# Kernel optimization log

Hardware: AMD Instinct MI355X
Metric: run time of the kernel (lower is better)

The kernel has to match this reference:

```python
import jax, jax.numpy as jnp
import numpy as np

N_NODES = 100000
N_EDGES = 3200000
F_IN = 512
F_HID = 16
F_OUT = 40


def setup_inputs() -> dict:
    key = jax.random.key(0)
    k_x, k_e, k_w1, k_w2 = jax.random.split(key, 4)
    x = jax.random.normal(k_x, (N_NODES, F_IN), dtype=jnp.float32)
    edge_index = jax.random.randint(k_e, (2, N_EDGES), 0, N_NODES, dtype=jnp.int32)
    # Glorot-ish init for GCN weights
    W1 = jax.random.normal(k_w1, (F_IN, F_HID), dtype=jnp.float32) * (1.0 / np.sqrt(F_IN))
    b1 = jnp.zeros((F_HID,), dtype=jnp.float32)
    W2 = jax.random.normal(k_w2, (F_HID, F_OUT), dtype=jnp.float32) * (1.0 / np.sqrt(F_HID))
    b2 = jnp.zeros((F_OUT,), dtype=jnp.float32)
    return {"x": x, "edge_index": edge_index, "W1": W1, "b1": b1, "W2": W2, "b2": b2}


def reference(x, edge_index, W1, b1, W2, b2):
    # Eval-mode forward: dropout is identity.
    n = x.shape[0]
    loops = jnp.arange(n, dtype=edge_index.dtype)
    row = jnp.concatenate([edge_index[0], loops])  # sources (incl. self-loops)
    col = jnp.concatenate([edge_index[1], loops])  # targets
    # Symmetric GCN normalization: deg^{-1/2}[row] * deg^{-1/2}[col]
    deg = jax.ops.segment_sum(jnp.ones_like(row, dtype=x.dtype), col, num_segments=n)
    dinv = jnp.where(deg > 0, jax.lax.rsqrt(deg), 0.0).astype(x.dtype)
    norm = dinv[row] * dinv[col]  # [E+N]

    def gcn_conv(h, W, b):
        h = h @ W                                   # [N, F_out] dense transform first
        msg = h[row] * norm[:, None]                # gather + scale
        return jax.ops.segment_sum(msg, col, num_segments=n) + b  # scatter-add

    h = jax.nn.relu(gcn_conv(x, W1, b1))
    out = gcn_conv(h, W2, b2)
    return jax.nn.log_softmax(out, axis=1)
```

## Files before the change

kernel.cpp:

```cpp
#include <hip/hip_runtime.h>
#include <hip/hip_bf16.h>

#define F_IN  512
#define F_HID 16
#define F_OUT 40
#define CH    8192

typedef __attribute__((ext_vector_type(4))) float f32x4;
typedef __attribute__((ext_vector_type(8))) short s16x8;
typedef unsigned short ushort_t;
typedef unsigned int uint_t;

__device__ __forceinline__ float lof(uint_t v) { return __uint_as_float(v << 16); }
__device__ __forceinline__ float hif(uint_t v) { return __uint_as_float(v & 0xffff0000u); }
__device__ __forceinline__ ushort_t f2bf(float f) {
    __hip_bfloat16 h = __float2bfloat16(f);
    union { __hip_bfloat16 h; ushort_t u; } v; v.h = h; return v.u;
}


__global__ __launch_bounds__(1024) void k_bhist(const int* __restrict__ col,
                                                int* __restrict__ bhall, int nE) {
    __shared__ int bh[256];
    int t = threadIdx.x;
    if (t < 256) bh[t] = 0;
    __syncthreads();
    int base = blockIdx.x * CH;
    int end  = min(base + CH, nE);
    for (int e = base + t; e < end; e += 1024)
        atomicAdd(&bh[col[e] >> 9], 1);
    __syncthreads();
    if (t < 256) bhall[blockIdx.x * 256 + t] = bh[t];
}

__global__ void k_bscan2(const int* __restrict__ bhall, int* __restrict__ bstart,
                         int* __restrict__ bcur, int nwge) {
    __shared__ int s[256];
    int t = threadIdx.x;
    int sum = 0;
    for (int w = 0; w < nwge; ++w) sum += bhall[w * 256 + t];
    s[t] = sum;
    __syncthreads();
    for (int off = 1; off < 256; off <<= 1) {
        int v = (t >= off) ? s[t - off] : 0;
        __syncthreads();
        s[t] += v;
        __syncthreads();
    }
    int ex = s[t] - sum;
    bstart[t] = ex;
    bcur[t] = ex;
    if (t == 255) bstart[256] = s[255];
}

__global__ __launch_bounds__(1024) void k_bscatter(const int* __restrict__ row,
                                                   const int* __restrict__ colv,
                                                   int* __restrict__ bcur,
                                                   int* __restrict__ pairs, int nE) {
    __shared__ int colS[CH];
    __shared__ int bh[256];
    __shared__ int lcur[256];
    int t = threadIdx.x;
    if (t < 256) bh[t] = 0;
    __syncthreads();
    int base = blockIdx.x * CH;
    int end  = min(base + CH, nE);
    for (int e = base + t; e < end; e += 1024) {
        int c = colv[e];
        colS[e - base] = c;
        atomicAdd(&bh[c >> 9], 1);
    }
    __syncthreads();
    if (t < 256) {
        int v = bh[t];
        if (v) lcur[t] = atomicAdd(&bcur[t], v);
    }
    __syncthreads();
    for (int e = base + t; e < end; e += 1024) {
        int c = colS[e - base];
        int pos = atomicAdd(&lcur[c >> 9], 1);
        pairs[pos] = (row[e] << 9) | (c & 511);
    }
}

__global__ __launch_bounds__(1024) void k_build(const int* __restrict__ bstart,
                                                const int* __restrict__ pairs,
                                                int* __restrict__ start,
                                                int* __restrict__ csr,
                                                float* __restrict__ dinv,
                                                int n, int nE) {
    __shared__ int h[512];
    __shared__ int s[512];
    __shared__ int cur[512];
    int t = threadIdx.x;
    if (t < 512) h[t] = 0;
    __syncthreads();
    int s0 = bstart[blockIdx.x], s1 = bstart[blockIdx.x + 1];
    for (int e = s0 + t; e < s1; e += 1024)
        atomicAdd(&h[pairs[e] & 511], 1);
    __syncthreads();
    if (t < 512) s[t] = h[t];
    __syncthreads();
    for (int off = 1; off < 512; off <<= 1) {
        int v = 0;
        if (t < 512 && t >= off) v = s[t - off];
        __syncthreads();
        if (t < 512) s[t] += v;
        __syncthreads();
    }
    if (t < 512) {
        int c = h[t];
        int st = s0 + s[t] - c;
        int node = (blockIdx.x << 9) + t;
        if (node < n) {
            start[node] = st;
            dinv[node] = rsqrtf((float)c + 1.0f);
        }
        cur[t] = st;
    }
    if (blockIdx.x == 0 && t == 0) start[n] = nE;
    __syncthreads();
    for (int e = s0 + t; e < s1; e += 1024) {
        int v = pairs[e];
        int pos = atomicAdd(&cur[v & 511], 1);
        csr[pos] = v >> 9;
    }
}

__global__ __launch_bounds__(256) void k_xw1(const float* __restrict__ x,
                                             const float* __restrict__ W1,
                                             const float* __restrict__ dinv,
                                             ushort_t* __restrict__ g1b, int n_tiles) {
    int lane = threadIdx.x & 63;
    int wid  = threadIdx.x >> 6;
    int m = lane & 15;
    int g = lane >> 4;

    s16x8 bf[16];
#pragma unroll
    for (int kb = 0; kb < 16; ++kb) {
        union { s16x8 s; unsigned u[4]; } bu;
#pragma unroll
        for (int p = 0; p < 4; ++p) {
            int k0 = kb * 32 + g * 8 + p * 2;
            float lo = W1[(k0 + 0) * F_HID + m];
            float hi = W1[(k0 + 1) * F_HID + m];
            unsigned pk;
            asm("v_cvt_pk_bf16_f32 %0, %1, %2" : "=v"(pk) : "v"(lo), "v"(hi));
            bu.u[p] = pk;
        }
        bf[kb] = bu.s;
    }

    int tile = blockIdx.x * 4 + wid;
    if (tile >= n_tiles) return;

    const float* xr = x + (size_t)(tile * 16 + m) * F_IN + g * 8;
    f32x4 acc = {0.f, 0.f, 0.f, 0.f};
#pragma unroll
    for (int kb = 0; kb < 16; ++kb) {
        f32x4 xa = *(const f32x4*)(xr + kb * 32);
        f32x4 xb = *(const f32x4*)(xr + kb * 32 + 4);
        union { s16x8 s; unsigned u[4]; } au;
        asm("v_cvt_pk_bf16_f32 %0, %1, %2" : "=v"(au.u[0]) : "v"(xa.x), "v"(xa.y));
        asm("v_cvt_pk_bf16_f32 %0, %1, %2" : "=v"(au.u[1]) : "v"(xa.z), "v"(xa.w));
        asm("v_cvt_pk_bf16_f32 %0, %1, %2" : "=v"(au.u[2]) : "v"(xb.x), "v"(xb.y));
        asm("v_cvt_pk_bf16_f32 %0, %1, %2" : "=v"(au.u[3]) : "v"(xb.z), "v"(xb.w));
        acc = __builtin_amdgcn_mfma_f32_16x16x32_bf16(au.s, bf[kb], acc, 0, 0, 0);
    }
#pragma unroll
    for (int p = 0; p < 4; ++p) {
        int rr = tile * 16 + g * 4 + p;
        g1b[(size_t)rr * F_HID + m] = f2bf(acc[p] * dinv[rr]);
    }
}

__global__ __launch_bounds__(256) void k_gather1(const int* __restrict__ start,
                                                 const int* __restrict__ csr,
                                                 const uint_t* __restrict__ g1,
                                                 const float* __restrict__ dinv,
                                                 const float* __restrict__ b1,
                                                 uint_t* __restrict__ g2, int n) {
    int wid = threadIdx.x >> 6, lane = threadIdx.x & 63;
    int node = blockIdx.x * 4 + wid;
    if (node >= n) return;
    int fp = lane & 7, sub = lane >> 3;
    int s0 = start[node], s1 = start[node + 1];
    int len = s1 - s0;
    int q = (len + 7) >> 3;
    int e = s0 + sub * q;
    int end = min(e + q, s1);
    float l0 = 0.f, h0 = 0.f, l1 = 0.f, h1 = 0.f, l2 = 0.f, h2 = 0.f, l3 = 0.f, h3 = 0.f;
    for (; e + 4 <= end; e += 4) {
        int r0 = csr[e], r1 = csr[e + 1], r2 = csr[e + 2], r3 = csr[e + 3];
        uint_t v0 = g1[r0 * 8 + fp], v1 = g1[r1 * 8 + fp];
        uint_t v2 = g1[r2 * 8 + fp], v3 = g1[r3 * 8 + fp];
        l0 += lof(v0); h0 += hif(v0);
        l1 += lof(v1); h1 += hif(v1);
        l2 += lof(v2); h2 += hif(v2);
        l3 += lof(v3); h3 += hif(v3);
    }
    for (; e < end; ++e) {
        uint_t v = g1[csr[e] * 8 + fp];
        l0 += lof(v); h0 += hif(v);
    }
    float alo = (l0 + l1) + (l2 + l3);
    float ahi = (h0 + h1) + (h2 + h3);
    alo += __shfl_xor(alo, 8);  ahi += __shfl_xor(ahi, 8);
    alo += __shfl_xor(alo, 16); ahi += __shfl_xor(ahi, 16);
    alo += __shfl_xor(alo, 32); ahi += __shfl_xor(ahi, 32);
    uint_t sv = g1[(size_t)node * 8 + fp];
    alo += lof(sv); ahi += hif(sv);
    float di = dinv[node];
    const float2* b1v = (const float2*)b1;
    float2 bb = b1v[fp];
    float hlo = fmaxf(di * alo + bb.x, 0.f) * di;
    float hhi = fmaxf(di * ahi + bb.y, 0.f) * di;
    if (sub == 0) {
        unsigned pk;
        asm("v_cvt_pk_bf16_f32 %0, %1, %2" : "=v"(pk) : "v"(hlo), "v"(hhi));
        g2[(size_t)node * 8 + fp] = pk;
    }
}

__global__ __launch_bounds__(256) void k_gather2f(const int* __restrict__ start,
                                                  const int* __restrict__ csr,
                                                  const uint_t* __restrict__ g2,
                                                  const float* __restrict__ dinv,
                                                  const float* __restrict__ W2,
                                                  const float* __restrict__ b2,
                                                  float* __restrict__ out, int n) {
    int wid = threadIdx.x >> 6, lane = threadIdx.x & 63;
    int node = blockIdx.x * 4 + wid;
    if (node >= n) return;
    int fp = lane & 7, sub = lane >> 3;
    int j = (lane < F_OUT) ? lane : 0;

    float w2c[F_HID];
#pragma unroll
    for (int k = 0; k < F_HID; ++k) w2c[k] = W2[k * F_OUT + j];
    float bj = b2[j];

    int s0 = start[node], s1 = start[node + 1];
    int len = s1 - s0;
    int q = (len + 7) >> 3;
    int e = s0 + sub * q;
    int end = min(e + q, s1);
    float l0 = 0.f, h0 = 0.f, l1 = 0.f, h1 = 0.f, l2 = 0.f, h2 = 0.f, l3 = 0.f, h3 = 0.f;
    for (; e + 4 <= end; e += 4) {
        int r0 = csr[e], r1 = csr[e + 1], r2 = csr[e + 2], r3 = csr[e + 3];
        uint_t v0 = g2[r0 * 8 + fp], v1 = g2[r1 * 8 + fp];
        uint_t v2 = g2[r2 * 8 + fp], v3 = g2[r3 * 8 + fp];
        l0 += lof(v0); h0 += hif(v0);
        l1 += lof(v1); h1 += hif(v1);
        l2 += lof(v2); h2 += hif(v2);
        l3 += lof(v3); h3 += hif(v3);
    }
    for (; e < end; ++e) {
        uint_t v = g2[csr[e] * 8 + fp];
        l0 += lof(v); h0 += hif(v);
    }
    float alo = (l0 + l1) + (l2 + l3);
    float ahi = (h0 + h1) + (h2 + h3);
    alo += __shfl_xor(alo, 8);  ahi += __shfl_xor(ahi, 8);
    alo += __shfl_xor(alo, 16); ahi += __shfl_xor(ahi, 16);
    alo += __shfl_xor(alo, 32); ahi += __shfl_xor(ahi, 32);
    uint_t sv = g2[(size_t)node * 8 + fp];
    alo += lof(sv); ahi += hif(sv);
    float di = dinv[node];
    float a_lo = di * alo;
    float a_hi = di * ahi;

    float o = bj;
#pragma unroll
    for (int k = 0; k < F_HID; k += 2) {
        o += __shfl(a_lo, k >> 1) * w2c[k] + __shfl(a_hi, k >> 1) * w2c[k + 1];
    }

    float mo = (lane < F_OUT) ? o : -3.4e38f;
#pragma unroll
    for (int off = 32; off; off >>= 1) mo = fmaxf(mo, __shfl_xor(mo, off));
    float ev = (lane < F_OUT) ? __expf(o - mo) : 0.f;
    float sv2 = ev;
#pragma unroll
    for (int off = 32; off; off >>= 1) sv2 += __shfl_xor(sv2, off);
    float lse = mo + __logf(sv2);
    if (lane < F_OUT) out[(size_t)node * F_OUT + lane] = o - lse;
}


extern "C" void kernel_launch(void* const* d_in, const int* in_sizes, int n_in,
                              void* d_out, int out_size, void* d_ws, size_t ws_size,
                              hipStream_t stream) {
    const float* x  = (const float*)d_in[0];
    const int*   ei = (const int*)d_in[1];
    const float* W1 = (const float*)d_in[2];
    const float* b1 = (const float*)d_in[3];
    const float* W2 = (const float*)d_in[4];
    const float* b2 = (const float*)d_in[5];
    float* out = (float*)d_out;

    const int N = out_size / F_OUT;
    const int E = in_sizes[1] / 2;
    const int* row = ei;
    const int* col = ei + E;

    const int NBUCK = (N + 511) >> 9;
    const int NWGE  = (E + CH - 1) / CH;
    const int tiles = (N + 15) / 16;
    const int nbT   = (tiles + 3) / 4;
    const int nbG   = (N + 3) / 4;

    int* bstart   = (int*)d_ws;
    int* bcur     = bstart + 260;
    int* bhall    = bcur + 256;
    int* start    = bhall + NWGE * 256;
    int* csr      = start + N + 4;
    int* pairs    = csr + E;
    float* dinv   = (float*)(pairs + E);
    uint_t* g1    = (uint_t*)(dinv + N);
    uint_t* g2    = g1 + (size_t)N * 8;

    k_bhist<<<NWGE, 1024, 0, stream>>>(col, bhall, E);
    k_bscan2<<<1, 256, 0, stream>>>(bhall, bstart, bcur, NWGE);
    k_bscatter<<<NWGE, 1024, 0, stream>>>(row, col, bcur, pairs, E);
    k_build<<<NBUCK, 1024, 0, stream>>>(bstart, pairs, start, csr, dinv, N, E);

    k_xw1<<<nbT, 256, 0, stream>>>(x, W1, dinv, (ushort_t*)g1, tiles);

    k_gather1<<<nbG, 256, 0, stream>>>(start, csr, g1, dinv, b1, g2, N);
    k_gather2f<<<nbG, 256, 0, stream>>>(start, csr, g2, dinv, W2, b2, out, N);
}
```

Measured before the change: 257.6 us.

## Fuse X@W1 with edge histogram and apply dinv scaling in CSR build

Merges the dense X@W1 MFMA kernel into the first histogram launch, so the bandwidth-heavy transform of x runs alongside the edge-bucket histogram instead of after the CSR build. The dinv scaling of g1 moves into k_build, which rescales the bf16 rows in place. The two gather kernels become persistent, with a fixed grid of 2048 blocks and each wave looping over a contiguous run of nodes, reusing start[] boundaries between nodes. The in-place rescale adds a second bf16 rounding, and the persistent split can unbalance work when degrees vary.

```diff
diff --git a/kernel.cpp b/kernel.cpp
--- a/kernel.cpp
+++ b/kernel.cpp
@@ -18,19 +18,67 @@
     union { __hip_bfloat16 h; ushort_t u; } v; v.h = h; return v.u;
 }
 
-
-__global__ __launch_bounds__(1024) void k_bhist(const int* __restrict__ col,
-                                                int* __restrict__ bhall, int nE) {
+__global__ __launch_bounds__(512) void k_pre(const float* __restrict__ x,
+                                             const float* __restrict__ W1,
+                                             ushort_t* __restrict__ g1b,
+                                             const int* __restrict__ col,
+                                             int* __restrict__ bhall,
+                                             int n_tiles, int nbX, int nE) {
     __shared__ int bh[256];
     int t = threadIdx.x;
-    if (t < 256) bh[t] = 0;
-    __syncthreads();
-    int base = blockIdx.x * CH;
-    int end  = min(base + CH, nE);
-    for (int e = base + t; e < end; e += 1024)
-        atomicAdd(&bh[col[e] >> 9], 1);
-    __syncthreads();
-    if (t < 256) bhall[blockIdx.x * 256 + t] = bh[t];
+    if ((int)blockIdx.x < nbX) {
+        int lane = t & 63;
+        int wid  = t >> 6;
+        int m = lane & 15;
+        int g = lane >> 4;
+        int tile = blockIdx.x * 8 + wid;
+        if (tile >= n_tiles) return;
+
+        s16x8 bf[16];
+#pragma unroll
+        for (int kb = 0; kb < 16; ++kb) {
+            union { s16x8 s; unsigned u[4]; } bu;
+#pragma unroll
+            for (int p = 0; p < 4; ++p) {
+                int k0 = kb * 32 + g * 8 + p * 2;
+                float lo = W1[(k0 + 0) * F_HID + m];
+                float hi = W1[(k0 + 1) * F_HID + m];
+                unsigned pk;
+                asm("v_cvt_pk_bf16_f32 %0, %1, %2" : "=v"(pk) : "v"(lo), "v"(hi));
+                bu.u[p] = pk;
+            }
+            bf[kb] = bu.s;
+        }
+
+        const float* xr = x + (size_t)(tile * 16 + m) * F_IN + g * 8;
+        f32x4 acc = {0.f, 0.f, 0.f, 0.f};
+#pragma unroll
+        for (int kb = 0; kb < 16; ++kb) {
+            f32x4 xa = *(const f32x4*)(xr + kb * 32);
+            f32x4 xb = *(const f32x4*)(xr + kb * 32 + 4);
+            union { s16x8 s; unsigned u[4]; } au;
+            asm("v_cvt_pk_bf16_f32 %0, %1, %2" : "=v"(au.u[0]) : "v"(xa.x), "v"(xa.y));
+            asm("v_cvt_pk_bf16_f32 %0, %1, %2" : "=v"(au.u[1]) : "v"(xa.z), "v"(xa.w));
+            asm("v_cvt_pk_bf16_f32 %0, %1, %2" : "=v"(au.u[2]) : "v"(xb.x), "v"(xb.y));
+            asm("v_cvt_pk_bf16_f32 %0, %1, %2" : "=v"(au.u[3]) : "v"(xb.z), "v"(xb.w));
+            acc = __builtin_amdgcn_mfma_f32_16x16x32_bf16(au.s, bf[kb], acc, 0, 0, 0);
+        }
+#pragma unroll
+        for (int p = 0; p < 4; ++p) {
+            int rr = tile * 16 + g * 4 + p;
+            g1b[(size_t)rr * F_HID + m] = f2bf(acc[p]);
+        }
+    } else {
+        int b = blockIdx.x - nbX;
+        if (t < 256) bh[t] = 0;
+        __syncthreads();
+        int base = b * CH;
+        int end  = min(base + CH, nE);
+        for (int e = base + t; e < end; e += 512)
+            atomicAdd(&bh[col[e] >> 9], 1);
+        __syncthreads();
+        if (t < 256) bhall[b * 256 + t] = bh[t];
+    }
 }
 
 __global__ void k_bscan2(const int* __restrict__ bhall, int* __restrict__ bstart,
@@ -88,10 +136,12 @@
                                                 int* __restrict__ start,
                                                 int* __restrict__ csr,
                                                 float* __restrict__ dinv,
+                                                uint_t* __restrict__ g1,
                                                 int n, int nE) {
     __shared__ int h[512];
     __shared__ int s[512];
     __shared__ int cur[512];
+    __shared__ float dv[512];
     int t = threadIdx.x;
     if (t < 512) h[t] = 0;
     __syncthreads();
@@ -108,70 +158,38 @@
         if (t < 512) s[t] += v;
         __syncthreads();
     }
+    int nbase = blockIdx.x << 9;
     if (t < 512) {
         int c = h[t];
         int st = s0 + s[t] - c;
-        int node = (blockIdx.x << 9) + t;
+        int node = nbase + t;
+        float d = rsqrtf((float)c + 1.0f);
+        if (node < n) { start[node] = st; dinv[node] = d; }
+        dv[t] = d;
+        cur[t] = st;
+    }
+    if (blockIdx.x == 0 && t == 0) start[n] = nE;
+    __syncthreads();
+    {
+        int nl = t >> 1;
+        int node = nbase + nl;
         if (node < n) {
-            start[node] = st;
-            dinv[node] = rsqrtf((float)c + 1.0f);
-        }
-        cur[t] = st;
-    }
-    if (blockIdx.x == 0 && t == 0) start[n] = nE;
-    __syncthreads();
+            float d = dv[nl];
+            uint_t* gp = g1 + (size_t)node * 8 + (t & 1) * 4;
+#pragma unroll
+            for (int i = 0; i < 4; ++i) {
+                uint_t v = gp[i];
+                float lo = lof(v) * d, hi = hif(v) * d;
+                unsigned pk;
+                asm("v_cvt_pk_bf16_f32 %0, %1, %2" : "=v"(pk) : "v"(lo), "v"(hi));
+                gp[i] = pk;
+            }
+        }
+    }
     for (int e = s0 + t; e < s1; e += 1024) {
         int v = pairs[e];
         int pos = atomicAdd(&cur[v & 511], 1);
         csr[pos] = v >> 9;
-    }
-}
-
-__global__ __launch_bounds__(256) void k_xw1(const float* __restrict__ x,
-                                             const float* __restrict__ W1,
-                                             const float* __restrict__ dinv,
-                                             ushort_t* __restrict__ g1b, int n_tiles) {
-    int lane = threadIdx.x & 63;
-    int wid  = threadIdx.x >> 6;
-    int m = lane & 15;
-    int g = lane >> 4;
-
-    s16x8 bf[16];
-#pragma unroll
-    for (int kb = 0; kb < 16; ++kb) {
-        union { s16x8 s; unsigned u[4]; } bu;
-#pragma unroll
-        for (int p = 0; p < 4; ++p) {
-            int k0 = kb * 32 + g * 8 + p * 2;
-            float lo = W1[(k0 + 0) * F_HID + m];
-            float hi = W1[(k0 + 1) * F_HID + m];
-            unsigned pk;
-            asm("v_cvt_pk_bf16_f32 %0, %1, %2" : "=v"(pk) : "v"(lo), "v"(hi));
-            bu.u[p] = pk;
-        }
-        bf[kb] = bu.s;
-    }
-
-    int tile = blockIdx.x * 4 + wid;
-    if (tile >= n_tiles) return;
-
-    const float* xr = x + (size_t)(tile * 16 + m) * F_IN + g * 8;
-    f32x4 acc = {0.f, 0.f, 0.f, 0.f};
-#pragma unroll
-    for (int kb = 0; kb < 16; ++kb) {
-        f32x4 xa = *(const f32x4*)(xr + kb * 32);
-        f32x4 xb = *(const f32x4*)(xr + kb * 32 + 4);
-        union { s16x8 s; unsigned u[4]; } au;
-        asm("v_cvt_pk_bf16_f32 %0, %1, %2" : "=v"(au.u[0]) : "v"(xa.x), "v"(xa.y));
-        asm("v_cvt_pk_bf16_f32 %0, %1, %2" : "=v"(au.u[1]) : "v"(xa.z), "v"(xa.w));
-        asm("v_cvt_pk_bf16_f32 %0, %1, %2" : "=v"(au.u[2]) : "v"(xb.x), "v"(xb.y));
-        asm("v_cvt_pk_bf16_f32 %0, %1, %2" : "=v"(au.u[3]) : "v"(xb.z), "v"(xb.w));
-        acc = __builtin_amdgcn_mfma_f32_16x16x32_bf16(au.s, bf[kb], acc, 0, 0, 0);
-    }
-#pragma unroll
-    for (int p = 0; p < 4; ++p) {
-        int rr = tile * 16 + g * 4 + p;
-        g1b[(size_t)rr * F_HID + m] = f2bf(acc[p] * dinv[rr]);
     }
 }
 
@@ -180,46 +198,50 @@
                                                  const uint_t* __restrict__ g1,
                                                  const float* __restrict__ dinv,
                                                  const float* __restrict__ b1,
-                                                 uint_t* __restrict__ g2, int n) {
-    int wid = threadIdx.x >> 6, lane = threadIdx.x & 63;
-    int node = blockIdx.x * 4 + wid;
-    if (node >= n) return;
+                                                 uint_t* __restrict__ g2, int n, int npw) {
+    int gw = (blockIdx.x * 256 + threadIdx.x) >> 6;
+    int lane = threadIdx.x & 63;
     int fp = lane & 7, sub = lane >> 3;
-    int s0 = start[node], s1 = start[node + 1];
-    int len = s1 - s0;
-    int q = (len + 7) >> 3;
-    int e = s0 + sub * q;
-    int end = min(e + q, s1);
-    float l0 = 0.f, h0 = 0.f, l1 = 0.f, h1 = 0.f, l2 = 0.f, h2 = 0.f, l3 = 0.f, h3 = 0.f;
-    for (; e + 4 <= end; e += 4) {
-        int r0 = csr[e], r1 = csr[e + 1], r2 = csr[e + 2], r3 = csr[e + 3];
-        uint_t v0 = g1[r0 * 8 + fp], v1 = g1[r1 * 8 + fp];
-        uint_t v2 = g1[r2 * 8 + fp], v3 = g1[r3 * 8 + fp];
-        l0 += lof(v0); h0 += hif(v0);
-        l1 += lof(v1); h1 += hif(v1);
-        l2 += lof(v2); h2 += hif(v2);
-        l3 += lof(v3); h3 += hif(v3);
-    }
-    for (; e < end; ++e) {
-        uint_t v = g1[csr[e] * 8 + fp];
-        l0 += lof(v); h0 += hif(v);
-    }
-    float alo = (l0 + l1) + (l2 + l3);
-    float ahi = (h0 + h1) + (h2 + h3);
-    alo += __shfl_xor(alo, 8);  ahi += __shfl_xor(ahi, 8);
-    alo += __shfl_xor(alo, 16); ahi += __shfl_xor(ahi, 16);
-    alo += __shfl_xor(alo, 32); ahi += __shfl_xor(ahi, 32);
-    uint_t sv = g1[(size_t)node * 8 + fp];
-    alo += lof(sv); ahi += hif(sv);
-    float di = dinv[node];
-    const float2* b1v = (const float2*)b1;
-    float2 bb = b1v[fp];
-    float hlo = fmaxf(di * alo + bb.x, 0.f) * di;
-    float hhi = fmaxf(di * ahi + bb.y, 0.f) * di;
-    if (sub == 0) {
-        unsigned pk;
-        asm("v_cvt_pk_bf16_f32 %0, %1, %2" : "=v"(pk) : "v"(hlo), "v"(hhi));
-        g2[(size_t)node * 8 + fp] = pk;
+    int n0 = gw * npw, n1 = min(n0 + npw, n);
+    if (n0 >= n) return;
+    float2 bb = ((const float2*)b1)[fp];
+    int sA = start[n0];
+    for (int node = n0; node < n1; ++node) {
+        int sB = start[node + 1];
+        int len = sB - sA;
+        int q = (len + 7) >> 3;
+        int e = sA + sub * q;
+        int end = min(e + q, sB);
+        float l0 = 0.f, h0 = 0.f, l1 = 0.f, h1 = 0.f, l2 = 0.f, h2 = 0.f, l3 = 0.f, h3 = 0.f;
+        for (; e + 4 <= end; e += 4) {
+            int r0 = csr[e], r1 = csr[e + 1], r2 = csr[e + 2], r3 = csr[e + 3];
+            uint_t v0 = g1[r0 * 8 + fp], v1 = g1[r1 * 8 + fp];
+            uint_t v2 = g1[r2 * 8 + fp], v3 = g1[r3 * 8 + fp];
+            l0 += lof(v0); h0 += hif(v0);
+            l1 += lof(v1); h1 += hif(v1);
+            l2 += lof(v2); h2 += hif(v2);
+            l3 += lof(v3); h3 += hif(v3);
+        }
+        for (; e < end; ++e) {
+            uint_t v = g1[csr[e] * 8 + fp];
+            l0 += lof(v); h0 += hif(v);
+        }
+        float alo = (l0 + l1) + (l2 + l3);
+        float ahi = (h0 + h1) + (h2 + h3);
+        alo += __shfl_xor(alo, 8);  ahi += __shfl_xor(ahi, 8);
+        alo += __shfl_xor(alo, 16); ahi += __shfl_xor(ahi, 16);
+        alo += __shfl_xor(alo, 32); ahi += __shfl_xor(ahi, 32);
+        uint_t sv = g1[(size_t)node * 8 + fp];
+        alo += lof(sv); ahi += hif(sv);
+        float di = dinv[node];
+        float hlo = fmaxf(di * alo + bb.x, 0.f) * di;
+        float hhi = fmaxf(di * ahi + bb.y, 0.f) * di;
+        if (sub == 0) {
+            unsigned pk;
+            asm("v_cvt_pk_bf16_f32 %0, %1, %2" : "=v"(pk) : "v"(hlo), "v"(hhi));
+            g2[(size_t)node * 8 + fp] = pk;
+        }
+        sA = sB;
     }
 }
 
@@ -229,63 +251,67 @@
                                                   const float* __restrict__ dinv,
                                                   const float* __restrict__ W2,
                                                   const float* __restrict__ b2,
-                                                  float* __restrict__ out, int n) {
-    int wid = threadIdx.x >> 6, lane = threadIdx.x & 63;
-    int node = blockIdx.x * 4 + wid;
-    if (node >= n) return;
+                                                  float* __restrict__ out, int n, int npw) {
+    int gw = (blockIdx.x * 256 + threadIdx.x) >> 6;
+    int lane = threadIdx.x & 63;
     int fp = lane & 7, sub = lane >> 3;
+    int n0 = gw * npw, n1 = min(n0 + npw, n);
+    if (n0 >= n) return;
     int j = (lane < F_OUT) ? lane : 0;
-
     float w2c[F_HID];
 #pragma unroll
     for (int k = 0; k < F_HID; ++k) w2c[k] = W2[k * F_OUT + j];
     float bj = b2[j];
 
-    int s0 = start[node], s1 = start[node + 1];
-    int len = s1 - s0;
-    int q = (len + 7) >> 3;
-    int e = s0 + sub * q;
-    int end = min(e + q, s1);
-    float l0 = 0.f, h0 = 0.f, l1 = 0.f, h1 = 0.f, l2 = 0.f, h2 = 0.f, l3 = 0.f, h3 = 0.f;
-    for (; e + 4 <= end; e += 4) {
-        int r0 = csr[e], r1 = csr[e + 1], r2 = csr[e + 2], r3 = csr[e + 3];
-        uint_t v0 = g2[r0 * 8 + fp], v1 = g2[r1 * 8 + fp];
-        uint_t v2 = g2[r2 * 8 + fp], v3 = g2[r3 * 8 + fp];
-        l0 += lof(v0); h0 += hif(v0);
-        l1 += lof(v1); h1 += hif(v1);
-        l2 += lof(v2); h2 += hif(v2);
-        l3 += lof(v3); h3 += hif(v3);
-    }
-    for (; e < end; ++e) {
-        uint_t v = g2[csr[e] * 8 + fp];
-        l0 += lof(v); h0 += hif(v);
-    }
-    float alo = (l0 + l1) + (l2 + l3);
-    float ahi = (h0 + h1) + (h2 + h3);
-    alo += __shfl_xor(alo, 8);  ahi += __shfl_xor(ahi, 8);
-    alo += __shfl_xor(alo, 16); ahi += __shfl_xor(ahi, 16);
-    alo += __shfl_xor(alo, 32); ahi += __shfl_xor(ahi, 32);
-    uint_t sv = g2[(size_t)node * 8 + fp];
-    alo += lof(sv); ahi += hif(sv);
-    float di = dinv[node];
-    float a_lo = di * alo;
-    float a_hi = di * ahi;
-
-    float o = bj;
-#pragma unroll
-    for (int k = 0; k < F_HID; k += 2) {
-        o += __shfl(a_lo, k >> 1) * w2c[k] + __shfl(a_hi, k >> 1) * w2c[k + 1];
-    }
-
-    float mo = (lane < F_OUT) ? o : -3.4e38f;
-#pragma unroll
-    for (int off = 32; off; off >>= 1) mo = fmaxf(mo, __shfl_xor(mo, off));
-    float ev = (lane < F_OUT) ? __expf(o - mo) : 0.f;
-    float sv2 = ev;
-#pragma unroll
-    for (int off = 32; off; off >>= 1) sv2 += __shfl_xor(sv2, off);
-    float lse = mo + __logf(sv2);
-    if (lane < F_OUT) out[(size_t)node * F_OUT + lane] = o - lse;
+    int sA = start[n0];
+    for (int node = n0; node < n1; ++node) {
+        int sB = start[node + 1];
+        int len = sB - sA;
+        int q = (len + 7) >> 3;
+        int e = sA + sub * q;
+        int end = min(e + q, sB);
+        float l0 = 0.f, h0 = 0.f, l1 = 0.f, h1 = 0.f, l2 = 0.f, h2 = 0.f, l3 = 0.f, h3 = 0.f;
+        for (; e + 4 <= end; e += 4) {
+            int r0 = csr[e], r1 = csr[e + 1], r2 = csr[e + 2], r3 = csr[e + 3];
+            uint_t v0 = g2[r0 * 8 + fp], v1 = g2[r1 * 8 + fp];
+            uint_t v2 = g2[r2 * 8 + fp], v3 = g2[r3 * 8 + fp];
+            l0 += lof(v0); h0 += hif(v0);
+            l1 += lof(v1); h1 += hif(v1);
+            l2 += lof(v2); h2 += hif(v2);
+            l3 += lof(v3); h3 += hif(v3);
+        }
+        for (; e < end; ++e) {
+            uint_t v = g2[csr[e] * 8 + fp];
+            l0 += lof(v); h0 += hif(v);
+        }
+        float alo = (l0 + l1) + (l2 + l3);
+        float ahi = (h0 + h1) + (h2 + h3);
+        alo += __shfl_xor(alo, 8);  ahi += __shfl_xor(ahi, 8);
+        alo += __shfl_xor(alo, 16); ahi += __shfl_xor(ahi, 16);
+        alo += __shfl_xor(alo, 32); ahi += __shfl_xor(ahi, 32);
+        uint_t sv = g2[(size_t)node * 8 + fp];
+        alo += lof(sv); ahi += hif(sv);
+        float di = dinv[node];
+        float a_lo = di * alo;
+        float a_hi = di * ahi;
+
+        float o = bj;
+#pragma unroll
+        for (int k = 0; k < F_HID; k += 2) {
+            o += __shfl(a_lo, k >> 1) * w2c[k] + __shfl(a_hi, k >> 1) * w2c[k + 1];
+        }
+
+        float mo = (lane < F_OUT) ? o : -3.4e38f;
+#pragma unroll
+        for (int off = 32; off; off >>= 1) mo = fmaxf(mo, __shfl_xor(mo, off));
+        float ev = (lane < F_OUT) ? __expf(o - mo) : 0.f;
+        float sv2 = ev;
+#pragma unroll
+        for (int off = 32; off; off >>= 1) sv2 += __shfl_xor(sv2, off);
+        float lse = mo + __logf(sv2);
+        if (lane < F_OUT) out[(size_t)node * F_OUT + lane] = o - lse;
+        sA = sB;
+    }
 }
 
 
@@ -308,8 +334,9 @@
     const int NBUCK = (N + 511) >> 9;
     const int NWGE  = (E + CH - 1) / CH;
     const int tiles = (N + 15) / 16;
-    const int nbT   = (tiles + 3) / 4;
-    const int nbG   = (N + 3) / 4;
+    const int nbX   = (tiles + 7) / 8;
+    const int GBLK  = 2048;
+    const int npw   = (N + GBLK * 4 - 1) / (GBLK * 4);
 
     int* bstart   = (int*)d_ws;
     int* bcur     = bstart + 260;
@@ -321,13 +348,11 @@
     uint_t* g1    = (uint_t*)(dinv + N);
     uint_t* g2    = g1 + (size_t)N * 8;
 
-    k_bhist<<<NWGE, 1024, 0, stream>>>(col, bhall, E);
+    k_pre<<<nbX + NWGE, 512, 0, stream>>>(x, W1, (ushort_t*)g1, col, bhall, tiles, nbX, E);
     k_bscan2<<<1, 256, 0, stream>>>(bhall, bstart, bcur, NWGE);
     k_bscatter<<<NWGE, 1024, 0, stream>>>(row, col, bcur, pairs, E);
-    k_build<<<NBUCK, 1024, 0, stream>>>(bstart, pairs, start, csr, dinv, N, E);
-
-    k_xw1<<<nbT, 256, 0, stream>>>(x, W1, dinv, (ushort_t*)g1, tiles);
-
-    k_gather1<<<nbG, 256, 0, stream>>>(start, csr, g1, dinv, b1, g2, N);
-    k_gather2f<<<nbG, 256, 0, stream>>>(start, csr, g2, dinv, W2, b2, out, N);
-}
+    k_build<<<NBUCK, 1024, 0, stream>>>(bstart, pairs, start, csr, dinv, g1, N, E);
+
+    k_gather1<<<GBLK, 256, 0, stream>>>(start, csr, g1, dinv, b1, g2, N, npw);
+    k_gather2f<<<GBLK, 256, 0, stream>>>(start, csr, g2, dinv, W2, b2, out, N, npw);
+}
```

Result: slower. 278.8 us (+8.3%).
